# Performance work log

Hardware: AMD Instinct MI355X
Metric: run time of the kernel (lower is better)

Reference implementation:

```python
import jax, jax.numpy as jnp
import numpy as np

EPS = float(jnp.finfo(jnp.float32).eps)  # torch.nn.RMSNorm default eps for fp32
TOP_K = 2


def rmsnorm(x, w):
    return x * jax.lax.rsqrt(jnp.mean(x * x, axis=-1, keepdims=True) + EPS) * w


def setup_inputs() -> dict:
    B, T, D_IN, D_MODEL, D_FF, D_OUT, E = 8, 1024, 1024, 1024, 4096, 1024, 8
    STD = 0.02
    key = jax.random.key(0)
    ks = jax.random.split(key, 8)
    return {
        "s": jax.random.normal(ks[0], (B, T, D_IN), dtype=jnp.float32),
        "W_in": STD * jax.random.normal(ks[1], (D_MODEL, D_IN), dtype=jnp.float32),
        "in_norm_w": jnp.ones((D_MODEL,), dtype=jnp.float32),
        "Wr": STD * jax.random.normal(ks[2], (E, D_MODEL), dtype=jnp.float32),
        "expert_bias": jnp.zeros((E,), dtype=jnp.float32),
        "Wg": STD * jax.random.normal(ks[3], (E, D_FF, D_MODEL), dtype=jnp.float32),
        "Wu": STD * jax.random.normal(ks[4], (E, D_FF, D_MODEL), dtype=jnp.float32),
        "Wd": STD * jax.random.normal(ks[5], (E, D_MODEL, D_FF), dtype=jnp.float32),
        "enorm_w": jnp.ones((E, D_MODEL), dtype=jnp.float32),
        "out_norm_w": jnp.ones((D_MODEL,), dtype=jnp.float32),
        "W_out": STD * jax.random.normal(ks[6], (D_OUT, D_MODEL), dtype=jnp.float32),
    }


def reference(s, W_in, in_norm_w, Wr, expert_bias, Wg, Wu, Wd, enorm_w, out_norm_w, W_out):
    B, T, _ = s.shape
    x = s.reshape(B * T, -1)                      # (N, d_in)
    h = rmsnorm(x @ W_in.T, in_norm_w)            # (N, d_model)

    # --- top-k router (DeepSeek-style bias for selection, orig logits for gates) ---
    logits = h @ Wr.T                              # (N, E)
    _, idx = jax.lax.top_k(logits + expert_bias, TOP_K)   # (N, k)
    sel = jnp.take_along_axis(logits, idx, axis=-1)
    g_topk = jax.nn.softmax(sel, axis=-1)
    N = logits.shape[0]
    gates = jnp.zeros_like(logits).at[jnp.arange(N)[:, None], idx].set(g_topk)

    # --- experts: gates are exactly 0 for unselected experts, so the dense
    # weighted sum equals the original masked gather/scatter combine ---
    out = jnp.zeros_like(h)
    for e in range(Wg.shape[0]):
        gate = jax.nn.silu(h @ Wg[e].T)            # (N, d_ff)
        up = h @ Wu[e].T
        oe = rmsnorm((gate * up) @ Wd[e].T, enorm_w[e])
        out = out + gates[:, e:e + 1] * oe

    s_hat = rmsnorm(out, out_norm_w) @ W_out.T     # (N, d_out)
    return s_hat.reshape(B, T, -1)
```

## Files before the change

### kernel.cpp

```cpp
#include <hip/hip_runtime.h>


#define NT      8192
#define DMODEL  1024
#define DFF     4096
#define NEXP    8
#define MAXROWS (NT * 2 + NEXP * 256)
#define RMS_EPS 1.1920928955078125e-07f

typedef __attribute__((ext_vector_type(8))) short bf16x8;
typedef __attribute__((ext_vector_type(4))) float f32x4;

__device__ __forceinline__ float bf2f(unsigned short u) {
  union { unsigned int i; float f; } c; c.i = ((unsigned int)u) << 16; return c.f;
}
__device__ __forceinline__ unsigned short f2bf(float f) {
  union { float f; unsigned int i; } c; c.f = f;
  unsigned int x = c.i;
  return (unsigned short)((x + 0x7FFFu + ((x >> 16) & 1u)) >> 16);
}

#define BARX() __builtin_amdgcn_s_barrier()
#define LGKM0() do { asm volatile("s_waitcnt lgkmcnt(0)" ::: "memory"); \
                     __builtin_amdgcn_sched_barrier(0); } while (0)
#define VMC(n)  do { asm volatile("s_waitcnt vmcnt(" #n ")" ::: "memory"); \
                     __builtin_amdgcn_sched_barrier(0); } while (0)

__global__ __launch_bounds__(256) void cast_bf16_kernel(
    const float* __restrict__ src, unsigned short* __restrict__ dst, long n) {
  long i = ((long)blockIdx.x * 256 + threadIdx.x) * 4;
  const long stride = (long)gridDim.x * 1024;
  for (; i < n; i += stride) {
    float4 v = *(const float4*)(src + i);
    ushort4 o;
    o.x = f2bf(v.x); o.y = f2bf(v.y); o.z = f2bf(v.z); o.w = f2bf(v.w);
    *(ushort4*)(dst + i) = o;
  }
}

__device__ __forceinline__ void async_cp16(const void* g, void* l) {
  __builtin_amdgcn_global_load_lds((const __attribute__((address_space(1))) void*)g,
                                   (__attribute__((address_space(3))) void*)l, 16, 0, 0);
}

template <int FUSED, int GROUPED>
__global__ __launch_bounds__(512, 2) void gemm8ph(
    const unsigned short* __restrict__ A,
    const unsigned short* __restrict__ W0,
    const unsigned short* __restrict__ W1,
    void* __restrict__ Cv, void* __restrict__ Cv2,
    const int* __restrict__ offs,
    int K, int KT, size_t wstride) {
  const int gx = gridDim.x;
  const int nwg = gx * gridDim.y;
  int bid = blockIdx.y * gx + blockIdx.x;
  {
    const int q = nwg >> 3, r = nwg & 7;
    const int x = bid & 7, l = bid >> 3;
    bid = (x < r ? x * (q + 1) : r * (q + 1) + (x - r) * q) + l;
  }
  const int bx = bid % gx, by = bid / gx;

  const int row0 = bx * 256;
  int e = 0;
  if constexpr (GROUPED) {
    if (row0 >= offs[NEXP]) return;
#pragma unroll
    for (int i = 1; i < NEXP; ++i) e += (row0 >= offs[i]) ? 1 : 0;
  }

  __shared__ __align__(16) unsigned short lds[65536];

  const int t = threadIdx.x;
  const int lane = t & 63;
  const int wave = t >> 6;
  const int wm = wave >> 2, wn = wave & 3;
  const int lm = lane & 15, kq = lane >> 4;
  const int k0 = blockIdx.z * (KT << 6);

  const unsigned short* aP[2];
  const unsigned short* bP[2];
  int dl[2];
#pragma unroll
  for (int q = 0; q < 2; ++q) {
    const int L = q * 512 + t;
    const int row = L >> 2;
    const int kp = (t & 3) ^ ((row >> 1) & 3);
    dl[q] = L * 8;
    aP[q] = A + (size_t)(row0 + row) * K + kp * 8 + k0;
    if (FUSED) {
      const int f = by * 128 + ((row >> 6) << 5) + (row & 31);
      const unsigned short* wb = (row & 32) ? W1 : W0;
      bP[q] = wb + (size_t)e * wstride + (size_t)f * K + kp * 8 + k0;
    } else {
      bP[q] = W0 + (size_t)e * wstride + (size_t)(by * 256 + row) * K + kp * 8 + k0;
    }
  }

  int afo[8], bfo[4];
#pragma unroll
  for (int mi = 0; mi < 8; ++mi) {
    const int r = wm * 128 + mi * 16 + lm;
    afo[mi] = r * 32 + ((kq ^ ((r >> 1) & 3)) << 3);
  }
#pragma unroll
  for (int ni = 0; ni < 4; ++ni) {
    const int r = wn * 64 + ni * 16 + lm;
    bfo[ni] = 16384 + r * 32 + ((kq ^ ((r >> 1) & 3)) << 3);
  }

  f32x4 acc[8][4];
#pragma unroll
  for (int i = 0; i < 8; ++i)
#pragma unroll
    for (int j = 0; j < 4; ++j) acc[i][j] = (f32x4){0.f, 0.f, 0.f, 0.f};

  auto STG = [&](int tau, int ks, int isB) {
    const int roff = ((tau & 1) << 15) + (isB << 14) + (ks << 13);
    const int koff = (tau << 6) + (ks << 5);
#pragma unroll
    for (int q = 0; q < 2; ++q)
      async_cp16((isB ? bP[q] : aP[q]) + koff, lds + roff + dl[q]);
  };

  STG(0, 0, 0); STG(0, 0, 1); STG(0, 1, 0); STG(0, 1, 1);
  STG(1, 0, 0); STG(1, 0, 1); STG(1, 1, 0);
  VMC(6);
  BARX();

  for (int tau = 0; tau < KT; ++tau) {
    const int tb = (tau & 1) << 15;
    const bool s1 = (tau + 1 < KT), s2 = (tau + 2 < KT);
    bf16x8 af[8], bq0, bq1;

#pragma unroll
    for (int mi = 0; mi < 8; ++mi) af[mi] = *(const bf16x8*)(lds + tb + afo[mi]);
    bq0 = *(const bf16x8*)(lds + tb + bfo[0]);
    bq1 = *(const bf16x8*)(lds + tb + bfo[1]);
    if (s1) STG(tau + 1, 1, 1);
    BARX(); LGKM0();
    __builtin_amdgcn_s_setprio(1);
#pragma unroll
    for (int mi = 0; mi < 8; ++mi) {
      acc[mi][0] = __builtin_amdgcn_mfma_f32_16x16x32_bf16(af[mi], bq0, acc[mi][0], 0, 0, 0);
      acc[mi][1] = __builtin_amdgcn_mfma_f32_16x16x32_bf16(af[mi], bq1, acc[mi][1], 0, 0, 0);
    }
    __builtin_amdgcn_s_setprio(0);
    BARX();

    bq0 = *(const bf16x8*)(lds + tb + bfo[2]);
    bq1 = *(const bf16x8*)(lds + tb + bfo[3]);
    if (s2) STG(tau + 2, 0, 0);
    BARX(); LGKM0();
    __builtin_amdgcn_s_setprio(1);
#pragma unroll
    for (int mi = 0; mi < 8; ++mi) {
      acc[mi][2] = __builtin_amdgcn_mfma_f32_16x16x32_bf16(af[mi], bq0, acc[mi][2], 0, 0, 0);
      acc[mi][3] = __builtin_amdgcn_mfma_f32_16x16x32_bf16(af[mi], bq1, acc[mi][3], 0, 0, 0);
    }
    __builtin_amdgcn_s_setprio(0);
    BARX();

#pragma unroll
    for (int mi = 0; mi < 8; ++mi) af[mi] = *(const bf16x8*)(lds + tb + 8192 + afo[mi]);
    bq0 = *(const bf16x8*)(lds + tb + 8192 + bfo[0]);
    bq1 = *(const bf16x8*)(lds + tb + 8192 + bfo[1]);
    if (s2) STG(tau + 2, 0, 1);
    BARX(); LGKM0();
    __builtin_amdgcn_s_setprio(1);
#pragma unroll
    for (int mi = 0; mi < 8; ++mi) {
      acc[mi][0] = __builtin_amdgcn_mfma_f32_16x16x32_bf16(af[mi], bq0, acc[mi][0], 0, 0, 0);
      acc[mi][1] = __builtin_amdgcn_mfma_f32_16x16x32_bf16(af[mi], bq1, acc[mi][1], 0, 0, 0);
    }
    __builtin_amdgcn_s_setprio(0);
    BARX();

    bq0 = *(const bf16x8*)(lds + tb + 8192 + bfo[2]);
    bq1 = *(const bf16x8*)(lds + tb + 8192 + bfo[3]);
    if (s2) STG(tau + 2, 1, 0);
    BARX(); LGKM0();
    __builtin_amdgcn_s_setprio(1);
#pragma unroll
    for (int mi = 0; mi < 8; ++mi) {
      acc[mi][2] = __builtin_amdgcn_mfma_f32_16x16x32_bf16(af[mi], bq0, acc[mi][2], 0, 0, 0);
      acc[mi][3] = __builtin_amdgcn_mfma_f32_16x16x32_bf16(af[mi], bq1, acc[mi][3], 0, 0, 0);
    }
    __builtin_amdgcn_s_setprio(0);
    if (tau + 3 <= KT) { VMC(6); }
    else if (tau + 2 == KT) { VMC(0); }
    BARX();
  }

  const long rbase = (long)row0 + wm * 128 + kq * 4;
  if (FUSED) {
    unsigned short* Hc = (unsigned short*)Cv;
    const int cb = by * 128 + wn * 32 + lm;
#pragma unroll
    for (int mi = 0; mi < 8; ++mi)
#pragma unroll
      for (int ni = 0; ni < 2; ++ni)
#pragma unroll
        for (int rr = 0; rr < 4; ++rr) {
          const float g = acc[mi][ni][rr];
          const float u = acc[mi][ni + 2][rr];
          const float h = g / (1.f + expf(-g)) * u;
          Hc[(rbase + mi * 16 + rr) * (long)DFF + cb + ni * 16] = f2bf(h);
        }
  } else {
    float* Cp = blockIdx.z ? (float*)Cv2 : (float*)Cv;
    const int cb = by * 256 + wn * 64 + lm;
#pragma unroll
    for (int mi = 0; mi < 8; ++mi)
#pragma unroll
      for (int ni = 0; ni < 4; ++ni)
#pragma unroll
        for (int rr = 0; rr < 4; ++rr)
          Cp[(rbase + mi * 16 + rr) * (long)DMODEL + cb + ni * 16] = acc[mi][ni][rr];
  }
}

__global__ __launch_bounds__(256) void rmsnorm_kernel(
    const float* __restrict__ in, const float* __restrict__ w,
    unsigned short* __restrict__ out, float* __restrict__ invrms) {
  const int row = blockIdx.x;
  const int tid = threadIdx.x;
  const float4 xv = ((const float4*)(in + (long)row * DMODEL))[tid];
  float ss = xv.x * xv.x + xv.y * xv.y + xv.z * xv.z + xv.w * xv.w;
#pragma unroll
  for (int o = 32; o > 0; o >>= 1) ss += __shfl_xor(ss, o);
  __shared__ float red[4];
  if ((tid & 63) == 0) red[tid >> 6] = ss;
  __syncthreads();
  const float tot = red[0] + red[1] + red[2] + red[3];
  const float s = rsqrtf(tot * (1.f / DMODEL) + RMS_EPS);
  if (invrms != nullptr && tid == 0) invrms[row] = s;
  const float4 wv = ((const float4*)w)[tid];
  ushort4 o4;
  o4.x = f2bf(xv.x * s * wv.x);
  o4.y = f2bf(xv.y * s * wv.y);
  o4.z = f2bf(xv.z * s * wv.z);
  o4.w = f2bf(xv.w * s * wv.w);
  ((ushort4*)(out + (long)row * DMODEL))[tid] = o4;
}

__global__ __launch_bounds__(256) void router_prep_kernel(
    const float* __restrict__ Wr, const float* __restrict__ nw,
    const float* __restrict__ W_in, float* __restrict__ Wr2) {
  __shared__ float wr[NEXP * DMODEL];
  const int tid = threadIdx.x;
  for (int i = tid; i < NEXP * DMODEL; i += 256) wr[i] = Wr[i] * nw[i & (DMODEL - 1)];
  __syncthreads();
  const int kl = tid & 127;
  const int eb = (tid >> 7) * 4;
  const int kg = blockIdx.x * 128 + kl;
  float a0 = 0.f, a1 = 0.f, a2 = 0.f, a3 = 0.f;
  for (int j = 0; j < DMODEL; ++j) {
    const float wij = W_in[(long)j * DMODEL + kg];
    a0 += wr[(eb + 0) * DMODEL + j] * wij;
    a1 += wr[(eb + 1) * DMODEL + j] * wij;
    a2 += wr[(eb + 2) * DMODEL + j] * wij;
    a3 += wr[(eb + 3) * DMODEL + j] * wij;
  }
  Wr2[(eb + 0) * DMODEL + kg] = a0;
  Wr2[(eb + 1) * DMODEL + kg] = a1;
  Wr2[(eb + 2) * DMODEL + kg] = a2;
  Wr2[(eb + 3) * DMODEL + kg] = a3;
}

__global__ __launch_bounds__(64) void router_kernel(
    const float* __restrict__ x, const float* __restrict__ Wr2,
    const float* __restrict__ bias, const float* __restrict__ invrms,
    int* __restrict__ cnt, int* __restrict__ tok,
    int* __restrict__ te, int2* __restrict__ ts, float2* __restrict__ tg) {
  const int row = blockIdx.x;
  const int lane = threadIdx.x;
  const float* xr = x + (long)row * DMODEL;
  float p[NEXP] = {0.f, 0.f, 0.f, 0.f, 0.f, 0.f, 0.f, 0.f};
  for (int k = lane; k < DMODEL; k += 64) {
    const float xv = xr[k];
#pragma unroll
    for (int e = 0; e < NEXP; ++e) p[e] += xv * Wr2[e * DMODEL + k];
  }
#pragma unroll
  for (int o = 32; o > 0; o >>= 1)
#pragma unroll
    for (int e = 0; e < NEXP; ++e) p[e] += __shfl_xor(p[e], o);
  if (lane == 0) {
    const float s = invrms[row];
    float logit[NEXP];
    float b0 = -1e30f, b1 = -1e30f;
    int i0 = 0, i1 = 0;
#pragma unroll
    for (int e = 0; e < NEXP; ++e) {
      logit[e] = p[e] * s;
      const float be = logit[e] + bias[e];
      if (be > b0)      { b1 = b0; i1 = i0; b0 = be; i0 = e; }
      else if (be > b1) { b1 = be; i1 = e; }
    }
    const float l0 = logit[i0], l1 = logit[i1];
    const float m = fmaxf(l0, l1);
    const float e0 = expf(l0 - m), e1 = expf(l1 - m);
    const float inv = 1.f / (e0 + e1);
    const int s0 = atomicAdd(&cnt[i0], 1);
    tok[i0 * NT + s0] = row;
    const int s1 = atomicAdd(&cnt[i1], 1);
    tok[i1 * NT + s1] = row;
    te[row] = i0 | (i1 << 8);
    ts[row] = make_int2(s0, s1);
    tg[row] = make_float2(e0 * inv, e1 * inv);
  }
}

__global__ __launch_bounds__(256) void pad_kernel(
    const int* __restrict__ cnt, int* __restrict__ tok, int* __restrict__ off) {
  __shared__ int sc[NEXP], sp[NEXP];
  const int tid = threadIdx.x;
  if (tid == 0) {
    int o = 0;
    for (int e = 0; e < NEXP; ++e) {
      const int c = cnt[e];
      const int p = (c + 255) & ~255;
      sc[e] = c; sp[e] = p;
      off[e] = o;
      o += p;
    }
    off[NEXP] = o;
  }
  __syncthreads();
  for (int e = 0; e < NEXP; ++e) {
    const int c = sc[e], p = sp[e];
    for (int s = c + tid; s < p; s += 256) tok[e * NT + s] = 0;
  }
}

__global__ __launch_bounds__(256) void gather_kernel(
    const unsigned short* __restrict__ hb, const int* __restrict__ tok,
    const int* __restrict__ offs, unsigned short* __restrict__ Ac) {
  const int r = blockIdx.x;
  if (r >= offs[NEXP]) return;
  int e = 0;
#pragma unroll
  for (int i = 1; i < NEXP; ++i) e += (r >= offs[i]) ? 1 : 0;
  const int src = tok[e * NT + (r - offs[e])];
  const ushort4* s4 = (const ushort4*)(hb + (long)src * DMODEL);
  ushort4* d4 = (ushort4*)(Ac + (long)r * DMODEL);
  d4[threadIdx.x] = s4[threadIdx.x];
}

__global__ __launch_bounds__(256) void combine_kernel(
    const float* __restrict__ oe0, const float* __restrict__ oe1,
    const float* __restrict__ enw, const float* __restrict__ outnw,
    const int* __restrict__ offs, const int* __restrict__ te,
    const int2* __restrict__ ts, const float2* __restrict__ tg,
    unsigned short* __restrict__ yb) {
  const int row = blockIdx.x;
  const int tid = threadIdx.x;
  const int pe = te[row];
  const int e0 = pe & 0xff, e1 = (pe >> 8) & 0xff;
  const int2 sl = ts[row];
  const float2 g = tg[row];
  const long r0 = (long)(offs[e0] + sl.x) * DMODEL;
  const long r1 = (long)(offs[e1] + sl.y) * DMODEL;

  float4 a = ((const float4*)(oe0 + r0))[tid];
  {
    const float4 b = ((const float4*)(oe1 + r0))[tid];
    a.x += b.x; a.y += b.y; a.z += b.z; a.w += b.w;
  }
  float4 c = ((const float4*)(oe0 + r1))[tid];
  {
    const float4 d = ((const float4*)(oe1 + r1))[tid];
    c.x += d.x; c.y += d.y; c.z += d.z; c.w += d.w;
  }
  float s0 = a.x * a.x + a.y * a.y + a.z * a.z + a.w * a.w;
  float s1 = c.x * c.x + c.y * c.y + c.z * c.z + c.w * c.w;
#pragma unroll
  for (int o = 32; o > 0; o >>= 1) {
    s0 += __shfl_xor(s0, o);
    s1 += __shfl_xor(s1, o);
  }
  __shared__ float red[8];
  if ((tid & 63) == 0) { red[tid >> 6] = s0; red[4 + (tid >> 6)] = s1; }
  __syncthreads();
  s0 = red[0] + red[1] + red[2] + red[3];
  s1 = red[4] + red[5] + red[6] + red[7];
  const float n0 = rsqrtf(s0 * (1.f / DMODEL) + RMS_EPS) * g.x;
  const float n1 = rsqrtf(s1 * (1.f / DMODEL) + RMS_EPS) * g.y;

  const float4 w0 = ((const float4*)(enw + (size_t)e0 * DMODEL))[tid];
  const float4 w1 = ((const float4*)(enw + (size_t)e1 * DMODEL))[tid];
  float4 v;
  v.x = a.x * n0 * w0.x + c.x * n1 * w1.x;
  v.y = a.y * n0 * w0.y + c.y * n1 * w1.y;
  v.z = a.z * n0 * w0.z + c.z * n1 * w1.z;
  v.w = a.w * n0 * w0.w + c.w * n1 * w1.w;

  float sv = v.x * v.x + v.y * v.y + v.z * v.z + v.w * v.w;
#pragma unroll
  for (int o = 32; o > 0; o >>= 1) sv += __shfl_xor(sv, o);
  __syncthreads();
  if ((tid & 63) == 0) red[tid >> 6] = sv;
  __syncthreads();
  sv = red[0] + red[1] + red[2] + red[3];
  const float so = rsqrtf(sv * (1.f / DMODEL) + RMS_EPS);

  const float4 wo = ((const float4*)outnw)[tid];
  ushort4 o4;
  o4.x = f2bf(v.x * so * wo.x);
  o4.y = f2bf(v.y * so * wo.y);
  o4.z = f2bf(v.z * so * wo.z);
  o4.w = f2bf(v.w * so * wo.w);
  ((ushort4*)(yb + (long)row * DMODEL))[tid] = o4;
}

extern "C" void kernel_launch(void* const* d_in, const int* in_sizes, int n_in,
                              void* d_out, int out_size, void* d_ws, size_t ws_size,
                              hipStream_t stream) {
  (void)in_sizes; (void)n_in; (void)out_size; (void)ws_size;
  const float* s_in  = (const float*)d_in[0];
  const float* W_in  = (const float*)d_in[1];
  const float* innw  = (const float*)d_in[2];
  const float* Wr    = (const float*)d_in[3];
  const float* ebias = (const float*)d_in[4];
  const float* Wg    = (const float*)d_in[5];
  const float* Wu    = (const float*)d_in[6];
  const float* Wd    = (const float*)d_in[7];
  const float* enw   = (const float*)d_in[8];
  const float* outnw = (const float*)d_in[9];
  const float* W_out = (const float*)d_in[10];
  float* out = (float*)d_out;

  char* base = (char*)d_ws;
  size_t off_b = 0;
  auto alloc = [&](size_t bytes) -> char* {
    char* p = base + off_b;
    off_b += (bytes + 255) & ~(size_t)255;
    return p;
  };
  unsigned short* xb    = (unsigned short*)alloc((size_t)NT * DMODEL * 2);
  unsigned short* Winb  = (unsigned short*)alloc((size_t)DMODEL * DMODEL * 2);
  unsigned short* Wgb   = (unsigned short*)alloc((size_t)NEXP * DFF * DMODEL * 2);
  unsigned short* Wub   = (unsigned short*)alloc((size_t)NEXP * DFF * DMODEL * 2);
  unsigned short* Wdb   = (unsigned short*)alloc((size_t)NEXP * DMODEL * DFF * 2);
  unsigned short* Woutb = (unsigned short*)alloc((size_t)DMODEL * DMODEL * 2);
  float*          hpre  = (float*)alloc((size_t)NT * DMODEL * 4);
  unsigned short* hb    = (unsigned short*)alloc((size_t)NT * DMODEL * 2);
  float*          invr  = (float*)alloc((size_t)NT * 4);
  float*          Wr2   = (float*)alloc((size_t)NEXP * DMODEL * 4);
  int*            cnt   = (int*)alloc((size_t)NEXP * 4);
  int*            offs  = (int*)alloc((size_t)(NEXP + 1) * 4);
  int*            tok   = (int*)alloc((size_t)NEXP * NT * 4);
  int*            te    = (int*)alloc((size_t)NT * 4);
  int2*           ts    = (int2*)alloc((size_t)NT * 8);
  float2*         tg    = (float2*)alloc((size_t)NT * 8);
  unsigned short* Ac    = (unsigned short*)alloc((size_t)MAXROWS * DMODEL * 2);
  unsigned short* Hc    = (unsigned short*)alloc((size_t)MAXROWS * DFF * 2);
  float*          oec   = (float*)alloc((size_t)MAXROWS * DMODEL * 4);
  unsigned short* yb    = xb;
  float*          oec2  = (float*)Wgb;

  hipMemsetAsync(cnt, 0, NEXP * 4, stream);
  cast_bf16_kernel<<<2048, 256, 0, stream>>>(s_in, xb, (long)NT * DMODEL);
  cast_bf16_kernel<<<2048, 256, 0, stream>>>(W_in, Winb, (long)DMODEL * DMODEL);
  cast_bf16_kernel<<<2048, 256, 0, stream>>>(Wg, Wgb, (long)NEXP * DFF * DMODEL);
  cast_bf16_kernel<<<2048, 256, 0, stream>>>(Wu, Wub, (long)NEXP * DFF * DMODEL);
  cast_bf16_kernel<<<2048, 256, 0, stream>>>(Wd, Wdb, (long)NEXP * DMODEL * DFF);
  cast_bf16_kernel<<<2048, 256, 0, stream>>>(W_out, Woutb, (long)DMODEL * DMODEL);

  gemm8ph<0, 0><<<dim3(NT / 256, DMODEL / 256), 512, 0, stream>>>(
      xb, Winb, nullptr, hpre, nullptr, nullptr, DMODEL, DMODEL / 64, 0);
  rmsnorm_kernel<<<NT, 256, 0, stream>>>(hpre, innw, hb, invr);

  router_prep_kernel<<<DMODEL / 128, 256, 0, stream>>>(Wr, innw, W_in, Wr2);
  router_kernel<<<NT, 64, 0, stream>>>(s_in, Wr2, ebias, invr, cnt, tok, te, ts, tg);
  pad_kernel<<<1, 256, 0, stream>>>(cnt, tok, offs);

  gather_kernel<<<MAXROWS, 256, 0, stream>>>(hb, tok, offs, Ac);

  gemm8ph<1, 1><<<dim3(MAXROWS / 256, DFF / 128), 512, 0, stream>>>(
      Ac, Wgb, Wub, Hc, nullptr, offs, DMODEL, DMODEL / 64, (size_t)DFF * DMODEL);

  gemm8ph<0, 1><<<dim3(MAXROWS / 256, DMODEL / 256, 2), 512, 0, stream>>>(
      Hc, Wdb, nullptr, oec, oec2, offs, DFF, 32, (size_t)DMODEL * DFF);

  combine_kernel<<<NT, 256, 0, stream>>>(
      oec, oec2, enw, outnw, offs, te, ts, tg, yb);

  gemm8ph<0, 0><<<dim3(NT / 256, DMODEL / 256), 512, 0, stream>>>(
      yb, Woutb, nullptr, out, nullptr, nullptr, DMODEL, DMODEL / 64, 0);
}
```

Measured before the change: 1.375 ms.

## Fuse casts into one launch, split-K input GEMM, gather tokens inside grouped GEMM

The six fp32-to-bf16 cast launches become one grid-stride kernel that picks its source buffer from hard-coded offsets. The input projection GEMM is split over K into two partial outputs, which a new rmsnorm kernel sums, to put more workgroups on the device. The separate gather kernel and its Ac buffer are removed: the fused gate/up GEMM reads its A rows straight from hb through the token index table. This saves launch overhead and one round trip through memory, at the cost of an extra fp32 partial buffer and non-contiguous A row loads.

```diff
diff --git a/kernel.cpp b/kernel.cpp
--- a/kernel.cpp
+++ b/kernel.cpp
@@ -26,15 +26,28 @@
 #define VMC(n)  do { asm volatile("s_waitcnt vmcnt(" #n ")" ::: "memory"); \
                      __builtin_amdgcn_sched_barrier(0); } while (0)
 
-__global__ __launch_bounds__(256) void cast_bf16_kernel(
-    const float* __restrict__ src, unsigned short* __restrict__ dst, long n) {
+__global__ __launch_bounds__(256) void cast_all_kernel(
+    const float* __restrict__ s0, const float* __restrict__ s1,
+    const float* __restrict__ s2, const float* __restrict__ s3,
+    const float* __restrict__ s4, const float* __restrict__ s5,
+    unsigned short* __restrict__ d0, unsigned short* __restrict__ d1,
+    unsigned short* __restrict__ d2, unsigned short* __restrict__ d3,
+    unsigned short* __restrict__ d4, unsigned short* __restrict__ d5) {
   long i = ((long)blockIdx.x * 256 + threadIdx.x) * 4;
   const long stride = (long)gridDim.x * 1024;
-  for (; i < n; i += stride) {
-    float4 v = *(const float4*)(src + i);
-    ushort4 o;
-    o.x = f2bf(v.x); o.y = f2bf(v.y); o.z = f2bf(v.z); o.w = f2bf(v.w);
-    *(ushort4*)(dst + i) = o;
+  for (; i < 111149056L; i += stride) {
+    const float* s; unsigned short* d; long o;
+    if (i < 8388608L)        { s = s0; d = d0; o = 0L; }
+    else if (i < 9437184L)   { s = s1; d = d1; o = 8388608L; }
+    else if (i < 42991616L)  { s = s2; d = d2; o = 9437184L; }
+    else if (i < 76546048L)  { s = s3; d = d3; o = 42991616L; }
+    else if (i < 110100480L) { s = s4; d = d4; o = 76546048L; }
+    else                     { s = s5; d = d5; o = 110100480L; }
+    const long j = i - o;
+    float4 v = *(const float4*)(s + j);
+    ushort4 u;
+    u.x = f2bf(v.x); u.y = f2bf(v.y); u.z = f2bf(v.z); u.w = f2bf(v.w);
+    *(ushort4*)(d + j) = u;
   }
 }
 
@@ -43,13 +56,13 @@
                                    (__attribute__((address_space(3))) void*)l, 16, 0, 0);
 }
 
-template <int FUSED, int GROUPED>
+template <int FUSED, int GROUPED, int GATHER>
 __global__ __launch_bounds__(512, 2) void gemm8ph(
     const unsigned short* __restrict__ A,
     const unsigned short* __restrict__ W0,
     const unsigned short* __restrict__ W1,
     void* __restrict__ Cv, void* __restrict__ Cv2,
-    const int* __restrict__ offs,
+    const int* __restrict__ offs, const int* __restrict__ tokp,
     int K, int KT, size_t wstride) {
   const int gx = gridDim.x;
   const int nwg = gx * gridDim.y;
@@ -62,11 +75,12 @@
   const int bx = bid % gx, by = bid / gx;
 
   const int row0 = bx * 256;
-  int e = 0;
+  int e = 0, seg0 = 0;
   if constexpr (GROUPED) {
     if (row0 >= offs[NEXP]) return;
 #pragma unroll
     for (int i = 1; i < NEXP; ++i) e += (row0 >= offs[i]) ? 1 : 0;
+    seg0 = offs[e];
   }
 
   __shared__ __align__(16) unsigned short lds[65536];
@@ -87,7 +101,10 @@
     const int row = L >> 2;
     const int kp = (t & 3) ^ ((row >> 1) & 3);
     dl[q] = L * 8;
-    aP[q] = A + (size_t)(row0 + row) * K + kp * 8 + k0;
+    size_t ar;
+    if constexpr (GATHER) ar = (size_t)tokp[e * NT + (row0 + row - seg0)];
+    else                  ar = (size_t)(row0 + row);
+    aP[q] = A + ar * K + kp * 8 + k0;
     if (FUSED) {
       const int f = by * 128 + ((row >> 6) << 5) + (row & 31);
       const unsigned short* wb = (row & 32) ? W1 : W0;
@@ -220,12 +237,15 @@
   }
 }
 
-__global__ __launch_bounds__(256) void rmsnorm_kernel(
-    const float* __restrict__ in, const float* __restrict__ w,
+__global__ __launch_bounds__(256) void rmsnorm2_kernel(
+    const float* __restrict__ in0, const float* __restrict__ in1,
+    const float* __restrict__ w,
     unsigned short* __restrict__ out, float* __restrict__ invrms) {
   const int row = blockIdx.x;
   const int tid = threadIdx.x;
-  const float4 xv = ((const float4*)(in + (long)row * DMODEL))[tid];
+  float4 xv = ((const float4*)(in0 + (long)row * DMODEL))[tid];
+  const float4 yv = ((const float4*)(in1 + (long)row * DMODEL))[tid];
+  xv.x += yv.x; xv.y += yv.y; xv.z += yv.z; xv.w += yv.w;
   float ss = xv.x * xv.x + xv.y * xv.y + xv.z * xv.z + xv.w * xv.w;
 #pragma unroll
   for (int o = 32; o > 0; o >>= 1) ss += __shfl_xor(ss, o);
@@ -234,7 +254,7 @@
   __syncthreads();
   const float tot = red[0] + red[1] + red[2] + red[3];
   const float s = rsqrtf(tot * (1.f / DMODEL) + RMS_EPS);
-  if (invrms != nullptr && tid == 0) invrms[row] = s;
+  if (tid == 0) invrms[row] = s;
   const float4 wv = ((const float4*)w)[tid];
   ushort4 o4;
   o4.x = f2bf(xv.x * s * wv.x);
@@ -332,20 +352,6 @@
     const int c = sc[e], p = sp[e];
     for (int s = c + tid; s < p; s += 256) tok[e * NT + s] = 0;
   }
-}
-
-__global__ __launch_bounds__(256) void gather_kernel(
-    const unsigned short* __restrict__ hb, const int* __restrict__ tok,
-    const int* __restrict__ offs, unsigned short* __restrict__ Ac) {
-  const int r = blockIdx.x;
-  if (r >= offs[NEXP]) return;
-  int e = 0;
-#pragma unroll
-  for (int i = 1; i < NEXP; ++i) e += (r >= offs[i]) ? 1 : 0;
-  const int src = tok[e * NT + (r - offs[e])];
-  const ushort4* s4 = (const ushort4*)(hb + (long)src * DMODEL);
-  ushort4* d4 = (ushort4*)(Ac + (long)r * DMODEL);
-  d4[threadIdx.x] = s4[threadIdx.x];
 }
 
 __global__ __launch_bounds__(256) void combine_kernel(
@@ -444,7 +450,8 @@
   unsigned short* Wub   = (unsigned short*)alloc((size_t)NEXP * DFF * DMODEL * 2);
   unsigned short* Wdb   = (unsigned short*)alloc((size_t)NEXP * DMODEL * DFF * 2);
   unsigned short* Woutb = (unsigned short*)alloc((size_t)DMODEL * DMODEL * 2);
-  float*          hpre  = (float*)alloc((size_t)NT * DMODEL * 4);
+  float*          hpre0 = (float*)alloc((size_t)NT * DMODEL * 4);
+  float*          hpre1 = (float*)alloc((size_t)NT * DMODEL * 4);
   unsigned short* hb    = (unsigned short*)alloc((size_t)NT * DMODEL * 2);
   float*          invr  = (float*)alloc((size_t)NT * 4);
   float*          Wr2   = (float*)alloc((size_t)NEXP * DMODEL * 4);
@@ -454,39 +461,33 @@
   int*            te    = (int*)alloc((size_t)NT * 4);
   int2*           ts    = (int2*)alloc((size_t)NT * 8);
   float2*         tg    = (float2*)alloc((size_t)NT * 8);
-  unsigned short* Ac    = (unsigned short*)alloc((size_t)MAXROWS * DMODEL * 2);
   unsigned short* Hc    = (unsigned short*)alloc((size_t)MAXROWS * DFF * 2);
   float*          oec   = (float*)alloc((size_t)MAXROWS * DMODEL * 4);
   unsigned short* yb    = xb;
   float*          oec2  = (float*)Wgb;
 
   hipMemsetAsync(cnt, 0, NEXP * 4, stream);
-  cast_bf16_kernel<<<2048, 256, 0, stream>>>(s_in, xb, (long)NT * DMODEL);
-  cast_bf16_kernel<<<2048, 256, 0, stream>>>(W_in, Winb, (long)DMODEL * DMODEL);
-  cast_bf16_kernel<<<2048, 256, 0, stream>>>(Wg, Wgb, (long)NEXP * DFF * DMODEL);
-  cast_bf16_kernel<<<2048, 256, 0, stream>>>(Wu, Wub, (long)NEXP * DFF * DMODEL);
-  cast_bf16_kernel<<<2048, 256, 0, stream>>>(Wd, Wdb, (long)NEXP * DMODEL * DFF);
-  cast_bf16_kernel<<<2048, 256, 0, stream>>>(W_out, Woutb, (long)DMODEL * DMODEL);
-
-  gemm8ph<0, 0><<<dim3(NT / 256, DMODEL / 256), 512, 0, stream>>>(
-      xb, Winb, nullptr, hpre, nullptr, nullptr, DMODEL, DMODEL / 64, 0);
-  rmsnorm_kernel<<<NT, 256, 0, stream>>>(hpre, innw, hb, invr);
+  cast_all_kernel<<<2048, 256, 0, stream>>>(
+      s_in, W_in, Wg, Wu, Wd, W_out, xb, Winb, Wgb, Wub, Wdb, Woutb);
+
+  gemm8ph<0, 0, 0><<<dim3(NT / 256, DMODEL / 256, 2), 512, 0, stream>>>(
+      xb, Winb, nullptr, hpre0, hpre1, nullptr, nullptr, DMODEL, 8, 0);
+  rmsnorm2_kernel<<<NT, 256, 0, stream>>>(hpre0, hpre1, innw, hb, invr);
 
   router_prep_kernel<<<DMODEL / 128, 256, 0, stream>>>(Wr, innw, W_in, Wr2);
   router_kernel<<<NT, 64, 0, stream>>>(s_in, Wr2, ebias, invr, cnt, tok, te, ts, tg);
   pad_kernel<<<1, 256, 0, stream>>>(cnt, tok, offs);
 
-  gather_kernel<<<MAXROWS, 256, 0, stream>>>(hb, tok, offs, Ac);
-
-  gemm8ph<1, 1><<<dim3(MAXROWS / 256, DFF / 128), 512, 0, stream>>>(
-      Ac, Wgb, Wub, Hc, nullptr, offs, DMODEL, DMODEL / 64, (size_t)DFF * DMODEL);
-
-  gemm8ph<0, 1><<<dim3(MAXROWS / 256, DMODEL / 256, 2), 512, 0, stream>>>(
-      Hc, Wdb, nullptr, oec, oec2, offs, DFF, 32, (size_t)DMODEL * DFF);
+  gemm8ph<1, 1, 1><<<dim3(MAXROWS / 256, DFF / 128), 512, 0, stream>>>(
+      hb, Wgb, Wub, Hc, nullptr, offs, tok, DMODEL, DMODEL / 64,
+      (size_t)DFF * DMODEL);
+
+  gemm8ph<0, 1, 0><<<dim3(MAXROWS / 256, DMODEL / 256, 2), 512, 0, stream>>>(
+      Hc, Wdb, nullptr, oec, oec2, offs, nullptr, DFF, 32, (size_t)DMODEL * DFF);
 
   combine_kernel<<<NT, 256, 0, stream>>>(
       oec, oec2, enw, outnw, offs, te, ts, tg, yb);
 
-  gemm8ph<0, 0><<<dim3(NT / 256, DMODEL / 256), 512, 0, stream>>>(
-      yb, Woutb, nullptr, out, nullptr, nullptr, DMODEL, DMODEL / 64, 0);
-}
+  gemm8ph<0, 0, 0><<<dim3(NT / 256, DMODEL / 256), 512, 0, stream>>>(
+      yb, Woutb, nullptr, out, nullptr, nullptr, nullptr, DMODEL, DMODEL / 64, 0);
+}
```

Result: no change. 1.366 ms (-0.7%).
